# Optimization experiments

Hardware: AMD Instinct MI355X
Metric: run time of the kernel (lower is better)

## Reference

```python
import jax, jax.numpy as jnp
import numpy as np

N = 100000      # nodes
E = 3200000     # edges (avg degree 32)
F = 256         # input features
C = 256         # output channels


def setup_inputs() -> dict:
    key = jax.random.key(0)
    k1, k2, k3, k4, k5 = jax.random.split(key, 5)
    x = jax.random.normal(k1, (N, F), dtype=jnp.float32)
    edge_row = jax.random.randint(k2, (E,), 0, N, dtype=jnp.int32)
    edge_col = jax.random.randint(k3, (E,), 0, N, dtype=jnp.int32)
    # precomputed normalized adjacency values (D^-1/2 (A+I) D^-1/2 entries)
    edge_vals = jax.random.uniform(k4, (E,), dtype=jnp.float32)
    kernel = jax.random.normal(k5, (F, C), dtype=jnp.float32) * (1.0 / np.sqrt(F))
    bias = jnp.zeros((C,), dtype=jnp.float32)
    return {"x": x, "edge_row": edge_row, "edge_col": edge_col,
            "edge_vals": edge_vals, "kernel": kernel, "bias": bias}


def reference(x, edge_row, edge_col, edge_vals, kernel, bias):
    # GraphConv: Z = relu( A_hat @ (X @ W) + b ), single mode, sparse A_hat.
    h = x @ kernel                                   # [N, C]
    msgs = edge_vals[:, None] * h[edge_col]          # [E, C] gather along cols
    agg = jax.ops.segment_sum(msgs, edge_row, num_segments=N)  # [N, C]
    return jax.nn.relu(agg + bias)
```

## Files before the change

### kernel.cpp

```cpp
#include <hip/hip_runtime.h>
#include <hip/hip_bf16.h>
#include <hip/hip_fp16.h>


#define BROWS 128
#define NBMAX 1024
#define CH_A1 16384
#define CH_A3 8192

typedef __attribute__((ext_vector_type(4))) float f32x4;
typedef __attribute__((ext_vector_type(8))) short s16x8;

__device__ __forceinline__ unsigned short f2bf(float f) {
    unsigned u = __float_as_uint(f);
    u += 0x7FFFu + ((u >> 16) & 1u);
    return (unsigned short)(u >> 16);
}

__global__ void k_wcvt(const float* __restrict__ W, unsigned short* __restrict__ Wt) {
    int idx = blockIdx.x * 256 + threadIdx.x;
    int k = idx >> 8, c = idx & 255;
    Wt[c * 256 + k] = f2bf(W[idx]);
}

__global__ __launch_bounds__(256) void kA1(const int* __restrict__ row,
                                           int* __restrict__ gcnt, int E, int NB) {
    __shared__ int h[NBMAX];
    int t = threadIdx.x;
    for (int j = t; j < NB; j += 256) h[j] = 0;
    __syncthreads();
    int start = blockIdx.x * CH_A1;
    int end = min(E, start + CH_A1);
    for (int i = start + t; i < end; i += 256)
        atomicAdd(&h[row[i] >> 7], 1);
    __syncthreads();
    for (int j = t; j < NB; j += 256)
        if (h[j]) atomicAdd(&gcnt[j], h[j]);
}

__global__ __launch_bounds__(1024) void kA2(const int* __restrict__ gcnt,
                                            int* __restrict__ bkt_base,
                                            int* __restrict__ gcur,
                                            int* __restrict__ rowptr,
                                            int NB, int N, int E) {
    __shared__ int s[1024];
    int t = threadIdx.x;
    int v = (t < NB) ? gcnt[t] : 0;
    s[t] = v;
    __syncthreads();
    for (int off = 1; off < 1024; off <<= 1) {
        int tmp = (t >= off) ? s[t - off] : 0;
        __syncthreads();
        if (t >= off) s[t] += tmp;
        __syncthreads();
    }
    if (t < NB) {
        int ex = s[t] - v;
        bkt_base[t] = ex;
        gcur[t] = ex;
    }
    if (t == 0) {
        bkt_base[NB] = E;
        rowptr[N] = E;
    }
}

__global__ __launch_bounds__(256) void kA3(const int* __restrict__ row,
                                           const int* __restrict__ col,
                                           const float* __restrict__ val,
                                           int* __restrict__ gcur,
                                           int2* __restrict__ binned,
                                           int E, int NB) {
    __shared__ int h[NBMAX];
    __shared__ int base[NBMAX];
    __shared__ int cur[NBMAX];
    int t = threadIdx.x;
    for (int j = t; j < NB; j += 256) { h[j] = 0; cur[j] = 0; }
    __syncthreads();
    int start = blockIdx.x * CH_A3;
    int end = min(E, start + CH_A3);
    for (int i = start + t; i < end; i += 256)
        atomicAdd(&h[row[i] >> 7], 1);
    __syncthreads();
    for (int j = t; j < NB; j += 256) {
        int c = h[j];
        base[j] = c ? atomicAdd(&gcur[j], c) : 0;
    }
    __syncthreads();
    for (int i = start + t; i < end; i += 256) {
        int r = row[i];
        int b = r >> 7;
        int ofs = atomicAdd(&cur[b], 1);
        unsigned hb = (unsigned)__half_as_ushort(__float2half(val[i]));
        binned[base[b] + ofs] = make_int2(col[i] | (int)(hb << 17), r & (BROWS - 1));
    }
}

__global__ __launch_bounds__(256) void kB(const int2* __restrict__ binned,
                                          const int* __restrict__ bkt_base,
                                          int* __restrict__ rowptr,
                                          unsigned* __restrict__ csr, int N) {
    __shared__ int cnt[BROWS];
    __shared__ int sc[BROWS];
    __shared__ int cur[BROWS];
    int t = threadIdx.x;
    int b = blockIdx.x;
    int r0 = b * BROWS;
    int bb = bkt_base[b];
    int be = bkt_base[b + 1];
    if (t < BROWS) cnt[t] = 0;
    __syncthreads();
    for (int i = bb + t; i < be; i += 256)
        atomicAdd(&cnt[binned[i].y], 1);
    __syncthreads();
    if (t < BROWS) sc[t] = cnt[t];
    __syncthreads();
    for (int off = 1; off < BROWS; off <<= 1) {
        int tmp = (t < BROWS && t >= off) ? sc[t - off] : 0;
        __syncthreads();
        if (t < BROWS && t >= off) sc[t] += tmp;
        __syncthreads();
    }
    if (t < BROWS) {
        int ex = sc[t] - cnt[t];
        cur[t] = ex;
        if (r0 + t < N) rowptr[r0 + t] = bb + ex;
    }
    __syncthreads();
    for (int i = bb + t; i < be; i += 256) {
        int2 e = binned[i];
        int ofs = atomicAdd(&cur[e.y], 1);
        csr[bb + ofs] = (unsigned)e.x;
    }
}

__global__ __launch_bounds__(256) void k_gemm(const float* __restrict__ X,
                                              const unsigned short* __restrict__ Wt,
                                              unsigned short* __restrict__ H, int M) {
    __shared__ unsigned short As[128][40];
    int t = threadIdx.x;
    int lane = t & 63;
    int w = t >> 6;
    int wm = w & 1, wn = w >> 1;
    int rb = blockIdx.x >> 2, cb = blockIdx.x & 3;
    int r0 = rb * 128, c0 = cb * 64;

    int srow = t >> 2;
    int sslot = t & 3;
    int gr0 = r0 + srow;        if (gr0 >= M) gr0 = M - 1;
    int gr1 = r0 + 64 + srow;   if (gr1 >= M) gr1 = M - 1;

    f32x4 acc[4][2] = {};

    for (int k0 = 0; k0 < 256; k0 += 32) {
        const float* p0 = &X[(size_t)gr0 * 256 + k0 + sslot * 8];
        const float* p1 = &X[(size_t)gr1 * 256 + k0 + sslot * 8];
        float4 a0 = *(const float4*)p0;
        float4 a1 = *(const float4*)(p0 + 4);
        float4 b0 = *(const float4*)p1;
        float4 b1 = *(const float4*)(p1 + 4);
        s16x8 va, vb;
        va[0] = (short)f2bf(a0.x); va[1] = (short)f2bf(a0.y);
        va[2] = (short)f2bf(a0.z); va[3] = (short)f2bf(a0.w);
        va[4] = (short)f2bf(a1.x); va[5] = (short)f2bf(a1.y);
        va[6] = (short)f2bf(a1.z); va[7] = (short)f2bf(a1.w);
        vb[0] = (short)f2bf(b0.x); vb[1] = (short)f2bf(b0.y);
        vb[2] = (short)f2bf(b0.z); vb[3] = (short)f2bf(b0.w);
        vb[4] = (short)f2bf(b1.x); vb[5] = (short)f2bf(b1.y);
        vb[6] = (short)f2bf(b1.z); vb[7] = (short)f2bf(b1.w);
        __syncthreads();
        *(s16x8*)&As[srow][sslot * 8] = va;
        *(s16x8*)&As[srow + 64][sslot * 8] = vb;
        __syncthreads();

        int kofs = (lane >> 4) * 8;
        s16x8 afr[4], bfr[2];
#pragma unroll
        for (int mi = 0; mi < 4; ++mi)
            afr[mi] = *(const s16x8*)&As[wm * 64 + mi * 16 + (lane & 15)][kofs];
#pragma unroll
        for (int ni = 0; ni < 2; ++ni) {
            int cn = c0 + wn * 32 + ni * 16 + (lane & 15);
            bfr[ni] = *(const s16x8*)&Wt[(size_t)cn * 256 + k0 + kofs];
        }
#pragma unroll
        for (int mi = 0; mi < 4; ++mi)
#pragma unroll
            for (int ni = 0; ni < 2; ++ni)
                acc[mi][ni] = __builtin_amdgcn_mfma_f32_16x16x32_bf16(
                    afr[mi], bfr[ni], acc[mi][ni], 0, 0, 0);
    }

#pragma unroll
    for (int mi = 0; mi < 4; ++mi) {
#pragma unroll
        for (int ni = 0; ni < 2; ++ni) {
            int rg = r0 + wm * 64 + mi * 16 + (lane >> 4) * 4;
            int cg = c0 + wn * 32 + ni * 16 + (lane & 15);
#pragma unroll
            for (int j = 0; j < 4; ++j) {
                if (rg + j < M)
                    H[(size_t)(rg + j) * 256 + cg] = f2bf(acc[mi][ni][j]);
            }
        }
    }
}

__global__ __launch_bounds__(256) void k_agg(const unsigned short* __restrict__ H,
                                             const int* __restrict__ rowptr,
                                             const unsigned* __restrict__ csr,
                                             const float* __restrict__ bias,
                                             float* __restrict__ out, int n) {
    int wave = threadIdx.x >> 6;
    int lane = threadIdx.x & 63;
    int node = blockIdx.x * 4 + wave;
    if (node >= n) return;
    int s = rowptr[node];
    int e = rowptr[node + 1];
    int cbase = lane * 4;

    float a0 = 0.f, a1 = 0.f, a2 = 0.f, a3 = 0.f;
    int i = s;
    for (; i + 3 < e; i += 4) {
        unsigned p0 = csr[i], p1 = csr[i + 1], p2 = csr[i + 2], p3 = csr[i + 3];
        ushort4 h0 = *(const ushort4*)&H[(p0 & 0x1FFFFu) * 256 + cbase];
        ushort4 h1 = *(const ushort4*)&H[(p1 & 0x1FFFFu) * 256 + cbase];
        ushort4 h2 = *(const ushort4*)&H[(p2 & 0x1FFFFu) * 256 + cbase];
        ushort4 h3 = *(const ushort4*)&H[(p3 & 0x1FFFFu) * 256 + cbase];
        float v0 = __half2float(__ushort_as_half((unsigned short)(p0 >> 17)));
        float v1 = __half2float(__ushort_as_half((unsigned short)(p1 >> 17)));
        float v2 = __half2float(__ushort_as_half((unsigned short)(p2 >> 17)));
        float v3 = __half2float(__ushort_as_half((unsigned short)(p3 >> 17)));
        a0 += v0 * __uint_as_float((unsigned)h0.x << 16);
        a1 += v0 * __uint_as_float((unsigned)h0.y << 16);
        a2 += v0 * __uint_as_float((unsigned)h0.z << 16);
        a3 += v0 * __uint_as_float((unsigned)h0.w << 16);
        a0 += v1 * __uint_as_float((unsigned)h1.x << 16);
        a1 += v1 * __uint_as_float((unsigned)h1.y << 16);
        a2 += v1 * __uint_as_float((unsigned)h1.z << 16);
        a3 += v1 * __uint_as_float((unsigned)h1.w << 16);
        a0 += v2 * __uint_as_float((unsigned)h2.x << 16);
        a1 += v2 * __uint_as_float((unsigned)h2.y << 16);
        a2 += v2 * __uint_as_float((unsigned)h2.z << 16);
        a3 += v2 * __uint_as_float((unsigned)h2.w << 16);
        a0 += v3 * __uint_as_float((unsigned)h3.x << 16);
        a1 += v3 * __uint_as_float((unsigned)h3.y << 16);
        a2 += v3 * __uint_as_float((unsigned)h3.z << 16);
        a3 += v3 * __uint_as_float((unsigned)h3.w << 16);
    }
    for (; i < e; ++i) {
        unsigned p0 = csr[i];
        ushort4 h0 = *(const ushort4*)&H[(p0 & 0x1FFFFu) * 256 + cbase];
        float v0 = __half2float(__ushort_as_half((unsigned short)(p0 >> 17)));
        a0 += v0 * __uint_as_float((unsigned)h0.x << 16);
        a1 += v0 * __uint_as_float((unsigned)h0.y << 16);
        a2 += v0 * __uint_as_float((unsigned)h0.z << 16);
        a3 += v0 * __uint_as_float((unsigned)h0.w << 16);
    }

    float4 b4 = *(const float4*)&bias[cbase];
    float4 o;
    o.x = fmaxf(a0 + b4.x, 0.f);
    o.y = fmaxf(a1 + b4.y, 0.f);
    o.z = fmaxf(a2 + b4.z, 0.f);
    o.w = fmaxf(a3 + b4.w, 0.f);
    *(float4*)&out[node * 256 + cbase] = o;
}

extern "C" void kernel_launch(void* const* d_in, const int* in_sizes, int n_in,
                              void* d_out, int out_size, void* d_ws, size_t ws_size,
                              hipStream_t stream) {
    const float* x     = (const float*)d_in[0];
    const int*   erow  = (const int*)d_in[1];
    const int*   ecol  = (const int*)d_in[2];
    const float* evals = (const float*)d_in[3];
    const float* W     = (const float*)d_in[4];
    const float* bias  = (const float*)d_in[5];
    float* out = (float*)d_out;

    const int C = 256;
    const int N = in_sizes[0] / C;
    const int E = in_sizes[1];
    const int NB = (N + BROWS - 1) / BROWS;

    char* ws = (char*)d_ws;
    size_t off = 0;
    auto carve = [&](size_t bytes) -> void* {
        void* p = ws + off;
        off += (bytes + 255) & ~(size_t)255;
        return p;
    };
    unsigned short* Hbf  = (unsigned short*)carve((size_t)N * C * 2);
    int2*           binned = (int2*)Hbf;
    unsigned*       csr  = (unsigned*)carve((size_t)E * 4);
    int*            rowp = (int*)carve((size_t)(N + 1) * 4);
    unsigned short* Wt   = (unsigned short*)carve((size_t)C * 256 * 2);
    int*            gcnt = (int*)carve((size_t)NB * 4);
    int*            gcur = (int*)carve((size_t)NB * 4);
    int*            bktb = (int*)carve((size_t)(NB + 1) * 4);

    hipMemsetAsync(gcnt, 0, (size_t)NB * 4, stream);
    k_wcvt<<<256, 256, 0, stream>>>(W, Wt);
    kA1<<<(E + CH_A1 - 1) / CH_A1, 256, 0, stream>>>(erow, gcnt, E, NB);
    kA2<<<1, 1024, 0, stream>>>(gcnt, bktb, gcur, rowp, NB, N, E);
    kA3<<<(E + CH_A3 - 1) / CH_A3, 256, 0, stream>>>(erow, ecol, evals, gcur,
                                                     binned, E, NB);
    kB<<<NB, 256, 0, stream>>>(binned, bktb, rowp, csr, N);

    int nRB = (N + 127) / 128;
    k_gemm<<<nRB * 4, 256, 0, stream>>>(x, Wt, Hbf, N);

    k_agg<<<(N + 3) / 4, 256, 0, stream>>>(Hbf, rowp, csr, bias, out, N);
}
```

Before: 442.1 us.

## Co-schedule CSR build with GEMM blocks and widen aggregation gathers

Merges the weight conversion into the histogram kernel. It splits the GEMM blocks across two hybrid kernels that also run the edge binning and the per-bucket CSR scatter, so the bandwidth-bound sort work and the compute-bound GEMM overlap on the GPU. To make this safe, binning now uses a separate workspace buffer when space allows, instead of aliasing H. The aggregation kernel now splits each wave into two half-waves that handle alternate edges with 16-byte gathers of 8 channels, then combines them with a cross-lane shuffle. The costs are extra workspace, heterogeneous blocks that may load-balance unevenly, and more registers in the aggregation kernel.

```diff
diff --git a/kernel.cpp b/kernel.cpp
--- a/kernel.cpp
+++ b/kernel.cpp
@@ -7,6 +7,7 @@
 #define NBMAX 1024
 #define CH_A1 16384
 #define CH_A3 8192
+#define GEMM_SMEM 10240
 
 typedef __attribute__((ext_vector_type(4))) float f32x4;
 typedef __attribute__((ext_vector_type(8))) short s16x8;
@@ -16,20 +17,27 @@
     u += 0x7FFFu + ((u >> 16) & 1u);
     return (unsigned short)(u >> 16);
 }
-
-__global__ void k_wcvt(const float* __restrict__ W, unsigned short* __restrict__ Wt) {
-    int idx = blockIdx.x * 256 + threadIdx.x;
-    int k = idx >> 8, c = idx & 255;
-    Wt[c * 256 + k] = f2bf(W[idx]);
-}
-
-__global__ __launch_bounds__(256) void kA1(const int* __restrict__ row,
-                                           int* __restrict__ gcnt, int E, int NB) {
+__device__ __forceinline__ float bf2f(unsigned short s) {
+    return __uint_as_float(((unsigned)s) << 16);
+}
+
+__global__ __launch_bounds__(256) void kA1h(const int* __restrict__ row,
+                                            int* __restrict__ gcnt,
+                                            const float* __restrict__ W,
+                                            unsigned short* __restrict__ Wt,
+                                            int E, int NB, int nHist) {
     __shared__ int h[NBMAX];
-    int t = threadIdx.x;
+    int bid = blockIdx.x;
+    int t = threadIdx.x;
+    if (bid >= nHist) {
+        int idx = (bid - nHist) * 256 + t;
+        int k = idx >> 8, c = idx & 255;
+        Wt[c * 256 + k] = f2bf(W[idx]);
+        return;
+    }
     for (int j = t; j < NB; j += 256) h[j] = 0;
     __syncthreads();
-    int start = blockIdx.x * CH_A1;
+    int start = bid * CH_A1;
     int end = min(E, start + CH_A1);
     for (int i = start + t; i < end; i += 256)
         atomicAdd(&h[row[i] >> 7], 1);
@@ -65,19 +73,19 @@
     }
 }
 
-__global__ __launch_bounds__(256) void kA3(const int* __restrict__ row,
-                                           const int* __restrict__ col,
-                                           const float* __restrict__ val,
-                                           int* __restrict__ gcur,
-                                           int2* __restrict__ binned,
-                                           int E, int NB) {
-    __shared__ int h[NBMAX];
-    __shared__ int base[NBMAX];
-    __shared__ int cur[NBMAX];
+__device__ __forceinline__ void a3_body(const int* __restrict__ row,
+                                        const int* __restrict__ col,
+                                        const float* __restrict__ val,
+                                        int* __restrict__ gcur,
+                                        int2* __restrict__ binned,
+                                        int E, int NB, int chunk, char* smem) {
+    int* h    = (int*)smem;
+    int* base = h + NB;
+    int* cur  = base + NB;
     int t = threadIdx.x;
     for (int j = t; j < NB; j += 256) { h[j] = 0; cur[j] = 0; }
     __syncthreads();
-    int start = blockIdx.x * CH_A3;
+    int start = chunk * CH_A3;
     int end = min(E, start + CH_A3);
     for (int i = start + t; i < end; i += 256)
         atomicAdd(&h[row[i] >> 7], 1);
@@ -96,15 +104,15 @@
     }
 }
 
-__global__ __launch_bounds__(256) void kB(const int2* __restrict__ binned,
-                                          const int* __restrict__ bkt_base,
-                                          int* __restrict__ rowptr,
-                                          unsigned* __restrict__ csr, int N) {
-    __shared__ int cnt[BROWS];
-    __shared__ int sc[BROWS];
-    __shared__ int cur[BROWS];
-    int t = threadIdx.x;
-    int b = blockIdx.x;
+__device__ __forceinline__ void kb_body(const int2* __restrict__ binned,
+                                        const int* __restrict__ bkt_base,
+                                        int* __restrict__ rowptr,
+                                        unsigned* __restrict__ csr,
+                                        int N, int b, char* smem) {
+    int* cnt = (int*)smem;
+    int* sc  = cnt + BROWS;
+    int* cur = sc + BROWS;
+    int t = threadIdx.x;
     int r0 = b * BROWS;
     int bb = bkt_base[b];
     int be = bkt_base[b + 1];
@@ -134,15 +142,17 @@
     }
 }
 
-__global__ __launch_bounds__(256) void k_gemm(const float* __restrict__ X,
-                                              const unsigned short* __restrict__ Wt,
-                                              unsigned short* __restrict__ H, int M) {
-    __shared__ unsigned short As[128][40];
+__device__ __forceinline__ void gemm_body(const float* __restrict__ X,
+                                          const unsigned short* __restrict__ Wt,
+                                          unsigned short* __restrict__ H,
+                                          int M, int g, char* smem) {
+    typedef unsigned short AsRow[40];
+    AsRow* As = (AsRow*)smem;
     int t = threadIdx.x;
     int lane = t & 63;
     int w = t >> 6;
     int wm = w & 1, wn = w >> 1;
-    int rb = blockIdx.x >> 2, cb = blockIdx.x & 3;
+    int rb = g >> 2, cb = g & 3;
     int r0 = rb * 128, c0 = cb * 64;
 
     int srow = t >> 2;
@@ -206,6 +216,44 @@
     }
 }
 
+__global__ __launch_bounds__(256) void hyb1(const int* __restrict__ row,
+                                            const int* __restrict__ col,
+                                            const float* __restrict__ val,
+                                            int* __restrict__ gcur,
+                                            int2* __restrict__ binned,
+                                            int E, int NB, int nA3,
+                                            const float* __restrict__ X,
+                                            const unsigned short* __restrict__ Wt,
+                                            unsigned short* __restrict__ H,
+                                            int M, int g0) {
+    extern __shared__ char smem[];
+    int bid = blockIdx.x;
+    if (bid < nA3) { a3_body(row, col, val, gcur, binned, E, NB, bid, smem); return; }
+    gemm_body(X, Wt, H, M, g0 + (bid - nA3), smem);
+}
+
+__global__ __launch_bounds__(256) void hyb2(const int2* __restrict__ binned,
+                                            const int* __restrict__ bktb,
+                                            int* __restrict__ rowptr,
+                                            unsigned* __restrict__ csr,
+                                            int N, int NB,
+                                            const float* __restrict__ X,
+                                            const unsigned short* __restrict__ Wt,
+                                            unsigned short* __restrict__ H,
+                                            int M, int g0) {
+    extern __shared__ char smem[];
+    int bid = blockIdx.x;
+    if (bid < NB) { kb_body(binned, bktb, rowptr, csr, N, bid, smem); return; }
+    gemm_body(X, Wt, H, M, g0 + (bid - NB), smem);
+}
+
+__global__ __launch_bounds__(256) void k_gemm_solo(const float* __restrict__ X,
+                                                   const unsigned short* __restrict__ Wt,
+                                                   unsigned short* __restrict__ H, int M) {
+    extern __shared__ char smem[];
+    gemm_body(X, Wt, H, M, blockIdx.x, smem);
+}
+
 __global__ __launch_bounds__(256) void k_agg(const unsigned short* __restrict__ H,
                                              const int* __restrict__ rowptr,
                                              const unsigned* __restrict__ csr,
@@ -217,54 +265,74 @@
     if (node >= n) return;
     int s = rowptr[node];
     int e = rowptr[node + 1];
-    int cbase = lane * 4;
-
-    float a0 = 0.f, a1 = 0.f, a2 = 0.f, a3 = 0.f;
+    int h = lane >> 5;
+    int cbase = (lane & 31) * 8;
+
+    float a0=0.f,a1=0.f,a2=0.f,a3=0.f,a4=0.f,a5=0.f,a6=0.f,a7=0.f;
+
+#define ACC(K, HV)                                                      \
+    {                                                                   \
+        float v = __half2float(__ushort_as_half((unsigned short)((K) >> 17))); \
+        a0 += v * bf2f((unsigned short)(HV)[0]);                        \
+        a1 += v * bf2f((unsigned short)(HV)[1]);                        \
+        a2 += v * bf2f((unsigned short)(HV)[2]);                        \
+        a3 += v * bf2f((unsigned short)(HV)[3]);                        \
+        a4 += v * bf2f((unsigned short)(HV)[4]);                        \
+        a5 += v * bf2f((unsigned short)(HV)[5]);                        \
+        a6 += v * bf2f((unsigned short)(HV)[6]);                        \
+        a7 += v * bf2f((unsigned short)(HV)[7]);                        \
+    }
+
     int i = s;
-    for (; i + 3 < e; i += 4) {
-        unsigned p0 = csr[i], p1 = csr[i + 1], p2 = csr[i + 2], p3 = csr[i + 3];
-        ushort4 h0 = *(const ushort4*)&H[(p0 & 0x1FFFFu) * 256 + cbase];
-        ushort4 h1 = *(const ushort4*)&H[(p1 & 0x1FFFFu) * 256 + cbase];
-        ushort4 h2 = *(const ushort4*)&H[(p2 & 0x1FFFFu) * 256 + cbase];
-        ushort4 h3 = *(const ushort4*)&H[(p3 & 0x1FFFFu) * 256 + cbase];
-        float v0 = __half2float(__ushort_as_half((unsigned short)(p0 >> 17)));
-        float v1 = __half2float(__ushort_as_half((unsigned short)(p1 >> 17)));
-        float v2 = __half2float(__ushort_as_half((unsigned short)(p2 >> 17)));
-        float v3 = __half2float(__ushort_as_half((unsigned short)(p3 >> 17)));
-        a0 += v0 * __uint_as_float((unsigned)h0.x << 16);
-        a1 += v0 * __uint_as_float((unsigned)h0.y << 16);
-        a2 += v0 * __uint_as_float((unsigned)h0.z << 16);
-        a3 += v0 * __uint_as_float((unsigned)h0.w << 16);
-        a0 += v1 * __uint_as_float((unsigned)h1.x << 16);
-        a1 += v1 * __uint_as_float((unsigned)h1.y << 16);
-        a2 += v1 * __uint_as_float((unsigned)h1.z << 16);
-        a3 += v1 * __uint_as_float((unsigned)h1.w << 16);
-        a0 += v2 * __uint_as_float((unsigned)h2.x << 16);
-        a1 += v2 * __uint_as_float((unsigned)h2.y << 16);
-        a2 += v2 * __uint_as_float((unsigned)h2.z << 16);
-        a3 += v2 * __uint_as_float((unsigned)h2.w << 16);
-        a0 += v3 * __uint_as_float((unsigned)h3.x << 16);
-        a1 += v3 * __uint_as_float((unsigned)h3.y << 16);
-        a2 += v3 * __uint_as_float((unsigned)h3.z << 16);
-        a3 += v3 * __uint_as_float((unsigned)h3.w << 16);
-    }
-    for (; i < e; ++i) {
-        unsigned p0 = csr[i];
-        ushort4 h0 = *(const ushort4*)&H[(p0 & 0x1FFFFu) * 256 + cbase];
-        float v0 = __half2float(__ushort_as_half((unsigned short)(p0 >> 17)));
-        a0 += v0 * __uint_as_float((unsigned)h0.x << 16);
-        a1 += v0 * __uint_as_float((unsigned)h0.y << 16);
-        a2 += v0 * __uint_as_float((unsigned)h0.z << 16);
-        a3 += v0 * __uint_as_float((unsigned)h0.w << 16);
-    }
-
-    float4 b4 = *(const float4*)&bias[cbase];
+    for (; i + 7 < e; i += 8) {
+        unsigned k0 = csr[i + h];
+        unsigned k1 = csr[i + 2 + h];
+        unsigned k2 = csr[i + 4 + h];
+        unsigned k3 = csr[i + 6 + h];
+        s16x8 h0 = *(const s16x8*)&H[(k0 & 0x1FFFFu) * 256 + cbase];
+        s16x8 h1 = *(const s16x8*)&H[(k1 & 0x1FFFFu) * 256 + cbase];
+        s16x8 h2 = *(const s16x8*)&H[(k2 & 0x1FFFFu) * 256 + cbase];
+        s16x8 h3 = *(const s16x8*)&H[(k3 & 0x1FFFFu) * 256 + cbase];
+        ACC(k0, h0); ACC(k1, h1); ACC(k2, h2); ACC(k3, h3);
+    }
+    for (; i + 1 < e; i += 2) {
+        unsigned k0 = csr[i + h];
+        s16x8 h0 = *(const s16x8*)&H[(k0 & 0x1FFFFu) * 256 + cbase];
+        ACC(k0, h0);
+    }
+    if (i < e) {
+        unsigned k0 = csr[i];
+        s16x8 h0 = *(const s16x8*)&H[(k0 & 0x1FFFFu) * 256 + cbase];
+        float v = h ? 0.f
+                    : __half2float(__ushort_as_half((unsigned short)(k0 >> 17)));
+        a0 += v * bf2f((unsigned short)h0[0]);
+        a1 += v * bf2f((unsigned short)h0[1]);
+        a2 += v * bf2f((unsigned short)h0[2]);
+        a3 += v * bf2f((unsigned short)h0[3]);
+        a4 += v * bf2f((unsigned short)h0[4]);
+        a5 += v * bf2f((unsigned short)h0[5]);
+        a6 += v * bf2f((unsigned short)h0[6]);
+        a7 += v * bf2f((unsigned short)h0[7]);
+    }
+#undef ACC
+
+    a0 += __shfl_xor(a0, 32); a1 += __shfl_xor(a1, 32);
+    a2 += __shfl_xor(a2, 32); a3 += __shfl_xor(a3, 32);
+    a4 += __shfl_xor(a4, 32); a5 += __shfl_xor(a5, 32);
+    a6 += __shfl_xor(a6, 32); a7 += __shfl_xor(a7, 32);
+
+    float w0 = h ? a4 : a0;
+    float w1 = h ? a5 : a1;
+    float w2 = h ? a6 : a2;
+    float w3 = h ? a7 : a3;
+    int cw = cbase + h * 4;
+    float4 b4 = *(const float4*)&bias[cw];
     float4 o;
-    o.x = fmaxf(a0 + b4.x, 0.f);
-    o.y = fmaxf(a1 + b4.y, 0.f);
-    o.z = fmaxf(a2 + b4.z, 0.f);
-    o.w = fmaxf(a3 + b4.w, 0.f);
-    *(float4*)&out[node * 256 + cbase] = o;
+    o.x = fmaxf(w0 + b4.x, 0.f);
+    o.y = fmaxf(w1 + b4.y, 0.f);
+    o.z = fmaxf(w2 + b4.z, 0.f);
+    o.w = fmaxf(w3 + b4.w, 0.f);
+    *(float4*)&out[node * 256 + cw] = o;
 }
 
 extern "C" void kernel_launch(void* const* d_in, const int* in_sizes, int n_in,
@@ -291,7 +359,6 @@
         return p;
     };
     unsigned short* Hbf  = (unsigned short*)carve((size_t)N * C * 2);
-    int2*           binned = (int2*)Hbf;
     unsigned*       csr  = (unsigned*)carve((size_t)E * 4);
     int*            rowp = (int*)carve((size_t)(N + 1) * 4);
     unsigned short* Wt   = (unsigned short*)carve((size_t)C * 256 * 2);
@@ -299,16 +366,32 @@
     int*            gcur = (int*)carve((size_t)NB * 4);
     int*            bktb = (int*)carve((size_t)(NB + 1) * 4);
 
+    bool fused = (off + (size_t)E * 8) <= ws_size;
+    int2* binned = fused ? (int2*)carve((size_t)E * 8) : (int2*)Hbf;
+
+    int nHist = (E + CH_A1 - 1) / CH_A1;
+    int nA3   = (E + CH_A3 - 1) / CH_A3;
+    int nRB   = (N + 127) / 128;
+    int gemmBlocks = nRB * 4;
+    int G1 = gemmBlocks / 2;
+    int G2 = gemmBlocks - G1;
+
     hipMemsetAsync(gcnt, 0, (size_t)NB * 4, stream);
-    k_wcvt<<<256, 256, 0, stream>>>(W, Wt);
-    kA1<<<(E + CH_A1 - 1) / CH_A1, 256, 0, stream>>>(erow, gcnt, E, NB);
+    kA1h<<<nHist + 256, 256, 0, stream>>>(erow, gcnt, W, Wt, E, NB, nHist);
     kA2<<<1, 1024, 0, stream>>>(gcnt, bktb, gcur, rowp, NB, N, E);
-    kA3<<<(E + CH_A3 - 1) / CH_A3, 256, 0, stream>>>(erow, ecol, evals, gcur,
-                                                     binned, E, NB);
-    kB<<<NB, 256, 0, stream>>>(binned, bktb, rowp, csr, N);
-
-    int nRB = (N + 127) / 128;
-    k_gemm<<<nRB * 4, 256, 0, stream>>>(x, Wt, Hbf, N);
+
+    if (fused) {
+        hyb1<<<nA3 + G1, 256, GEMM_SMEM, stream>>>(erow, ecol, evals, gcur, binned,
+                                                   E, NB, nA3, x, Wt, Hbf, N, 0);
+        hyb2<<<NB + G2, 256, GEMM_SMEM, stream>>>(binned, bktb, rowp, csr, N, NB,
+                                                  x, Wt, Hbf, N, G1);
+    } else {
+        hyb1<<<nA3, 256, GEMM_SMEM, stream>>>(erow, ecol, evals, gcur, binned,
+                                              E, NB, nA3, x, Wt, Hbf, N, 0);
+        hyb2<<<NB, 256, GEMM_SMEM, stream>>>(binned, bktb, rowp, csr, N, NB,
+                                             x, Wt, Hbf, N, 0);
+        k_gemm_solo<<<gemmBlocks, 256, GEMM_SMEM, stream>>>(x, Wt, Hbf, N);
+    }
 
     k_agg<<<(N + 3) / 4, 256, 0, stream>>>(Hbf, rowp, csr, bias, out, N);
 }
```

After: 435.6 us. About the same (-1.5%).
